# Kernel tuning notes

Measured on AMD Instinct MI355X. Metric: run time of the kernel, lower is better.

## Reference

```python
import jax, jax.numpy as jnp
import numpy as np

N_NODES = 100000
N_EDGES = 1600000
D_IN = 128
D_OUT = 256


def setup_inputs() -> dict:
    key = jax.random.key(0)
    k1, k2, k3 = jax.random.split(key, 3)
    H = jax.random.normal(k1, (N_NODES, D_IN), dtype=jnp.float32)
    edge_index = jax.random.randint(k2, (2, N_EDGES), 0, N_NODES, dtype=jnp.int64)
    # kaiming_normal_ on (in, out): fan computed over dim 1 -> std = sqrt(2/out)
    W = jax.random.normal(k3, (D_IN, D_OUT), dtype=jnp.float32) * np.sqrt(2.0 / D_OUT)
    return {"H": H, "edge_index": edge_index, "W": W}


def reference(H, edge_index, W):
    src, dst = edge_index[0], edge_index[1]
    # gather source node features per edge, scatter-add into destination nodes
    msgs = H[src]  # [E, D_IN]
    new_H = jax.ops.segment_sum(msgs, dst, num_segments=H.shape[0])  # [N, D_IN]
    out = H + new_H
    out = out @ W  # [N, D_OUT]
    return jax.nn.relu(out)
```

## Files before the change

### kernel.cpp

```cpp
#include <hip/hip_runtime.h>

#define N_NODES 100000
#define N_EDGES 1600000
#define D_IN    128
#define D_OUT   256
#define NB_SCAN ((N_NODES + 255) / 256)
#define BLK_ROWS 64
#define N_TILES  ((N_NODES + BLK_ROWS - 1) / BLK_ROWS)
#define X_ROWS   (N_TILES * BLK_ROWS)

#define NBUCK      98
#define BCAP       20480
#define BIN_CHUNK  1024
#define BIN_BLOCKS ((N_EDGES + BIN_CHUNK - 1) / BIN_CHUNK)

#define GBLK_ROWS  32
#define G_TILES    ((N_NODES + GBLK_ROWS - 1) / GBLK_ROWS)

typedef __attribute__((ext_vector_type(8))) short short8v;
typedef __attribute__((ext_vector_type(4))) float f32x4;

__device__ __forceinline__ unsigned bf16_rn(float f) {
    unsigned u = __float_as_uint(f);
    return (u + 0x7FFFu + ((u >> 16) & 1u)) >> 16;
}
__device__ __forceinline__ unsigned pack2_bf16(float a, float b) {
    return bf16_rn(a) | (bf16_rn(b) << 16);
}

__global__ void detect_idx64_kernel(const int* __restrict__ edge32,
                                    int* __restrict__ flag) {
    if (threadIdx.x == 0 && blockIdx.x == 0) {
        int is64 = 1;
        for (int i = 1; i < 32; i += 2) {
            if (edge32[i] != 0) { is64 = 0; break; }
        }
        *flag = is64;
    }
}

__device__ __forceinline__ int load_dst(const void* edge_raw, int is64, int e) {
    if (is64) return (int)((const long long*)edge_raw)[(long long)N_EDGES + e];
    return ((const int*)edge_raw)[N_EDGES + e];
}
__device__ __forceinline__ int load_src(const void* edge_raw, int is64, int e) {
    if (is64) return (int)((const long long*)edge_raw)[e];
    return ((const int*)edge_raw)[e];
}

__global__ __launch_bounds__(256) void cvt_h_kernel(
        const float* __restrict__ H, unsigned* __restrict__ Hb) {
    int i = blockIdx.x * 256 + threadIdx.x;
    if (i >= N_NODES * (D_IN / 2)) return;
    const float2 h = ((const float2*)H)[i];
    Hb[i] = pack2_bf16(h.x, h.y);
}

__global__ __launch_bounds__(256) void pack_w_kernel(
        const float* __restrict__ W, unsigned short* __restrict__ Wp) {
    int t = blockIdx.x * 256 + threadIdx.x;
    if (t >= 64 * 64) return;
    const int f  = t >> 6;
    const int l  = t & 63;
    const int nb = f >> 2;
    const int ks = f & 3;
    const int col  = nb * 16 + (l & 15);
    const int krow = ks * 32 + (l >> 4) * 8;
    #pragma unroll
    for (int i = 0; i < 8; ++i)
        Wp[(size_t)t * 8 + i] = (unsigned short)bf16_rn(W[(krow + i) * D_OUT + col]);
}

__global__ __launch_bounds__(256) void bin_hist_kernel(
        const void* __restrict__ edge_raw, const int* __restrict__ flag,
        int* __restrict__ bucket_alloc, int* __restrict__ binned) {
    __shared__ int cnt[128];
    __shared__ int gbase[128];
    const int tid = threadIdx.x;
    if (tid < 128) cnt[tid] = 0;
    __syncthreads();
    const int is64 = *flag;
    const int base = blockIdx.x * BIN_CHUNK + tid;

#define EDGE_A(i)                                                             \
    int rec##i = 0, pb##i = -1;                                               \
    {                                                                         \
        const int idx = base + (i) * 256;                                     \
        if (idx < N_EDGES) {                                                  \
            const int s = load_src(edge_raw, is64, idx);                      \
            const int d = load_dst(edge_raw, is64, idx);                      \
            if ((unsigned)s < N_NODES && (unsigned)d < N_NODES) {             \
                const int b = d >> 10;                                        \
                const int pos = atomicAdd(&cnt[b], 1);                        \
                rec##i = s | ((d & 1023) << 17);                              \
                pb##i  = pos | (b << 12);                                     \
            }                                                                 \
        }                                                                     \
    }
    EDGE_A(0) EDGE_A(1) EDGE_A(2) EDGE_A(3)
#undef EDGE_A

    __syncthreads();
    if (tid < NBUCK) gbase[tid] = atomicAdd(&bucket_alloc[tid], cnt[tid]);
    __syncthreads();

#define EDGE_B(i)                                                             \
    if (pb##i >= 0) {                                                         \
        const int b = pb##i >> 12;                                            \
        const int p = gbase[b] + (pb##i & 4095);                              \
        if (p < BCAP) binned[b * BCAP + p] = rec##i;                          \
    }
    EDGE_B(0) EDGE_B(1) EDGE_B(2) EDGE_B(3)
#undef EDGE_B
}

__global__ __launch_bounds__(128) void scan98_kernel(
        const int* __restrict__ bucket_alloc, int* __restrict__ segbase) {
    __shared__ int lds[128];
    const int t = threadIdx.x;
    lds[t] = (t < NBUCK) ? bucket_alloc[t] : 0;
    __syncthreads();
    for (int off = 1; off < 128; off <<= 1) {
        int u = (t >= off) ? lds[t - off] : 0;
        __syncthreads();
        lds[t] += u;
        __syncthreads();
    }
    if (t < NBUCK) segbase[t] = lds[t] - ((t < NBUCK) ? bucket_alloc[t] : 0);
}

__global__ __launch_bounds__(1024) void bucket_fill_scan_kernel(
        const int* __restrict__ bucket_alloc, const int* __restrict__ segbase,
        const int* __restrict__ binned,
        int* __restrict__ row_start, int* __restrict__ csr_pack) {
    __shared__ int hist[1024];
    const int b   = blockIdx.x;
    const int tid = threadIdx.x;
    hist[tid] = 0;
    __syncthreads();

    int cnt = bucket_alloc[b];
    if (cnt > BCAP) cnt = BCAP;
    const int base = b * BCAP;

    for (int p = tid; p < cnt; p += 1024)
        atomicAdd(&hist[(binned[base + p] >> 17) & 1023], 1);
    __syncthreads();

    const int myc = hist[tid];
    for (int off = 1; off < 1024; off <<= 1) {
        int u = (tid >= off) ? hist[tid - off] : 0;
        __syncthreads();
        hist[tid] += u;
        __syncthreads();
    }
    const int rs = segbase[b] + hist[tid] - myc;
    const int node = (b << 10) + tid;
    if (node <= N_NODES) row_start[node] = rs;

    hist[tid] = rs;
    __syncthreads();

    for (int p = tid; p < cnt; p += 1024) {
        const int rec = binned[base + p];
        const int dlo = (rec >> 17) & 1023;
        const int pos = atomicAdd(&hist[dlo], 1);
        csr_pack[pos] = (rec & 0x1FFFF) | ((dlo & 63) << 20);
    }
}

__global__ __launch_bounds__(256) void hist_kernel(
        const void* __restrict__ edge_raw, const int* __restrict__ flag,
        int* __restrict__ counts) {
    int e = blockIdx.x * blockDim.x + threadIdx.x;
    if (e >= N_EDGES) return;
    int dst = load_dst(edge_raw, *flag, e);
    if ((unsigned)dst < N_NODES) atomicAdd(&counts[dst], 1);
}

__global__ __launch_bounds__(256) void block_sum_kernel(
        const int* __restrict__ counts, int* __restrict__ bsum) {
    __shared__ int lds[256];
    int t = threadIdx.x;
    int i = blockIdx.x * 256 + t;
    lds[t] = (i < N_NODES) ? counts[i] : 0;
    __syncthreads();
    for (int off = 128; off > 0; off >>= 1) {
        if (t < off) lds[t] += lds[t + off];
        __syncthreads();
    }
    if (t == 0) bsum[blockIdx.x] = lds[0];
}

__global__ __launch_bounds__(512) void scan_bsum_kernel(
        int* __restrict__ bsum, int* __restrict__ row_start) {
    __shared__ int lds[512];
    int t = threadIdx.x;
    lds[t] = (t < NB_SCAN) ? bsum[t] : 0;
    __syncthreads();
    for (int off = 1; off < 512; off <<= 1) {
        int u = (t >= off) ? lds[t - off] : 0;
        __syncthreads();
        lds[t] += u;
        __syncthreads();
    }
    int excl = (t == 0) ? 0 : lds[t - 1];
    if (t < NB_SCAN) bsum[t] = excl;
    if (t == 0) row_start[N_NODES] = N_EDGES;
}

__global__ __launch_bounds__(256) void scan_counts_kernel(
        int* __restrict__ counts_cursor, const int* __restrict__ bsum,
        int* __restrict__ row_start) {
    __shared__ int lds[256];
    int t = threadIdx.x;
    int i = blockIdx.x * 256 + t;
    int c = (i < N_NODES) ? counts_cursor[i] : 0;
    lds[t] = c;
    __syncthreads();
    for (int off = 1; off < 256; off <<= 1) {
        int u = (t >= off) ? lds[t - off] : 0;
        __syncthreads();
        lds[t] += u;
        __syncthreads();
    }
    int rs = bsum[blockIdx.x] + lds[t] - c;
    if (i < N_NODES) {
        row_start[i] = rs;
        counts_cursor[i] = rs;
    }
}

__global__ __launch_bounds__(256) void fill_kernel(
        const void* __restrict__ edge_raw, const int* __restrict__ flag,
        int* __restrict__ cursor, int* __restrict__ csr_pack) {
    int e = blockIdx.x * blockDim.x + threadIdx.x;
    if (e >= N_EDGES) return;
    int is64 = *flag;
    int src = load_src(edge_raw, is64, e);
    int dst = load_dst(edge_raw, is64, e);
    if ((unsigned)dst >= N_NODES || (unsigned)src >= N_NODES) return;
    int pos = atomicAdd(&cursor[dst], 1);
    csr_pack[pos] = src | ((dst & 63) << 20);
}

__global__ __launch_bounds__(256) void gather_bf16_kernel(
        const float* __restrict__ H,
        const unsigned* __restrict__ Hb,
        const int* __restrict__ row_start,
        const int* __restrict__ csr_pack,
        unsigned* __restrict__ Xg) {
    __shared__ int idx_lds[4][256];

    const int gb   = blockIdx.x * GBLK_ROWS;
    const int tile = (gb >> 6) << 6;
    const int wv   = threadIdx.x >> 6;
    const int lane = threadIdx.x & 63;
    const int r0   = gb + wv * 8;
    if (r0 >= N_NODES) return;
    int r1 = r0 + 8; if (r1 > N_NODES) r1 = N_NODES;

    const int p0   = row_start[r0];
    const int pend = row_start[r1];

    for (int r = r0; r < r1; ++r) {
        if (row_start[r + 1] == row_start[r]) {
            const float2 h = ((const float2*)(H + (size_t)r * D_IN))[lane];
            __builtin_nontemporal_store(pack2_bf16(h.x, h.y),
                                        &Xg[(size_t)r * 64 + lane]);
        }
    }

    int    cur = -1;
    float2 acc = make_float2(0.f, 0.f);
    float2 hs  = make_float2(0.f, 0.f);

#define FLUSH()                                                               \
    __builtin_nontemporal_store(pack2_bf16(acc.x + hs.x, acc.y + hs.y),       \
                                &Xg[(size_t)(tile + cur) * 64 + lane]);

#define PROC(EV, UU)                                                          \
    {                                                                         \
        const int dl = (EV) >> 20;                                            \
        const float vx = __uint_as_float((UU) << 16);                         \
        const float vy = __uint_as_float((UU) & 0xFFFF0000u);                 \
        if (dl != cur) {                                                      \
            if (cur >= 0) { FLUSH(); }                                        \
            cur = dl;                                                         \
            hs  = ((const float2*)(H + (size_t)(tile + dl) * D_IN))[lane];    \
            acc = make_float2(vx, vy);                                        \
        } else {                                                              \
            acc.x += vx; acc.y += vy;                                         \
        }                                                                     \
    }

    for (int p = p0; p < pend; p += 256) {
        int m = pend - p;
        if (m > 256) m = 256;
        #pragma unroll
        for (int j = 0; j < 4; ++j) {
            const int o = lane + j * 64;
            if (o < m) idx_lds[wv][o] = csr_pack[p + o];
        }
        int n = 0;
        for (; n + 8 <= m; n += 8) {
            const int e0 = idx_lds[wv][n + 0];
            const int e1 = idx_lds[wv][n + 1];
            const int e2 = idx_lds[wv][n + 2];
            const int e3 = idx_lds[wv][n + 3];
            const int e4 = idx_lds[wv][n + 4];
            const int e5 = idx_lds[wv][n + 5];
            const int e6 = idx_lds[wv][n + 6];
            const int e7 = idx_lds[wv][n + 7];
            const unsigned u0 = Hb[(size_t)(e0 & 0xFFFFF) * 64 + lane];
            const unsigned u1 = Hb[(size_t)(e1 & 0xFFFFF) * 64 + lane];
            const unsigned u2 = Hb[(size_t)(e2 & 0xFFFFF) * 64 + lane];
            const unsigned u3 = Hb[(size_t)(e3 & 0xFFFFF) * 64 + lane];
            const unsigned u4 = Hb[(size_t)(e4 & 0xFFFFF) * 64 + lane];
            const unsigned u5 = Hb[(size_t)(e5 & 0xFFFFF) * 64 + lane];
            const unsigned u6 = Hb[(size_t)(e6 & 0xFFFFF) * 64 + lane];
            const unsigned u7 = Hb[(size_t)(e7 & 0xFFFFF) * 64 + lane];
            PROC(e0, u0) PROC(e1, u1) PROC(e2, u2) PROC(e3, u3)
            PROC(e4, u4) PROC(e5, u5) PROC(e6, u6) PROC(e7, u7)
        }
        for (; n < m; ++n) {
            const int e0 = idx_lds[wv][n];
            const unsigned u = Hb[(size_t)(e0 & 0xFFFFF) * 64 + lane];
            PROC(e0, u)
        }
    }
    if (cur >= 0) { FLUSH(); }
#undef PROC
#undef FLUSH
}

__global__ __launch_bounds__(256) void gather_f32_kernel(
        const float* __restrict__ H,
        const int* __restrict__ row_start,
        const int* __restrict__ csr_pack,
        unsigned* __restrict__ Xg) {
    __shared__ int idx_lds[4][256];

    const int gb   = blockIdx.x * GBLK_ROWS;
    const int tile = (gb >> 6) << 6;
    const int wv   = threadIdx.x >> 6;
    const int lane = threadIdx.x & 63;
    const int r0   = gb + wv * 8;
    if (r0 >= N_NODES) return;
    int r1 = r0 + 8; if (r1 > N_NODES) r1 = N_NODES;

    const int p0   = row_start[r0];
    const int pend = row_start[r1];

    for (int r = r0; r < r1; ++r) {
        if (row_start[r + 1] == row_start[r]) {
            const float2 h = ((const float2*)(H + (size_t)r * D_IN))[lane];
            Xg[(size_t)r * 64 + lane] = pack2_bf16(h.x, h.y);
        }
    }

    int    cur = -1;
    float2 acc = make_float2(0.f, 0.f);
    float2 hs  = make_float2(0.f, 0.f);

#define FLUSH() \
    Xg[(size_t)(tile + cur) * 64 + lane] = pack2_bf16(acc.x + hs.x, acc.y + hs.y);

#define PROC(EV, VV)                                                          \
    {                                                                         \
        const int dl = (EV) >> 20;                                            \
        if (dl != cur) {                                                      \
            if (cur >= 0) { FLUSH(); }                                        \
            cur = dl;                                                         \
            hs  = ((const float2*)(H + (size_t)(tile + dl) * D_IN))[lane];    \
            acc = (VV);                                                       \
        } else {                                                              \
            acc.x += (VV).x; acc.y += (VV).y;                                 \
        }                                                                     \
    }

    for (int p = p0; p < pend; p += 256) {
        int m = pend - p;
        if (m > 256) m = 256;
        #pragma unroll
        for (int j = 0; j < 4; ++j) {
            const int o = lane + j * 64;
            if (o < m) idx_lds[wv][o] = csr_pack[p + o];
        }
        int n = 0;
        for (; n + 8 <= m; n += 8) {
            const int e0 = idx_lds[wv][n + 0];
            const int e1 = idx_lds[wv][n + 1];
            const int e2 = idx_lds[wv][n + 2];
            const int e3 = idx_lds[wv][n + 3];
            const int e4 = idx_lds[wv][n + 4];
            const int e5 = idx_lds[wv][n + 5];
            const int e6 = idx_lds[wv][n + 6];
            const int e7 = idx_lds[wv][n + 7];
            const float2 v0 = ((const float2*)(H + (size_t)(e0 & 0xFFFFF) * D_IN))[lane];
            const float2 v1 = ((const float2*)(H + (size_t)(e1 & 0xFFFFF) * D_IN))[lane];
            const float2 v2 = ((const float2*)(H + (size_t)(e2 & 0xFFFFF) * D_IN))[lane];
            const float2 v3 = ((const float2*)(H + (size_t)(e3 & 0xFFFFF) * D_IN))[lane];
            const float2 v4 = ((const float2*)(H + (size_t)(e4 & 0xFFFFF) * D_IN))[lane];
            const float2 v5 = ((const float2*)(H + (size_t)(e5 & 0xFFFFF) * D_IN))[lane];
            const float2 v6 = ((const float2*)(H + (size_t)(e6 & 0xFFFFF) * D_IN))[lane];
            const float2 v7 = ((const float2*)(H + (size_t)(e7 & 0xFFFFF) * D_IN))[lane];
            PROC(e0, v0) PROC(e1, v1) PROC(e2, v2) PROC(e3, v3)
            PROC(e4, v4) PROC(e5, v5) PROC(e6, v6) PROC(e7, v7)
        }
        for (; n < m; ++n) {
            const int e0 = idx_lds[wv][n];
            const float2 v = ((const float2*)(H + (size_t)(e0 & 0xFFFFF) * D_IN))[lane];
            PROC(e0, v)
        }
    }
    if (cur >= 0) { FLUSH(); }
#undef PROC
#undef FLUSH
}

__global__ __launch_bounds__(256) void gemm_mfma_kernel(
        const unsigned* __restrict__ Xg,
        const unsigned short* __restrict__ Wp,
        float* __restrict__ out) {
    __shared__ unsigned Xs[64 * 64];

    const int tid = threadIdx.x;
    const int w   = tid >> 6;
    const int l   = tid & 63;
    const int g   = blockIdx.x * BLK_ROWS;

    #pragma unroll
    for (int j = 0; j < 4; ++j) {
        const int flat = j * 256 + tid;
        const int r   = flat >> 4;
        const int c16 = flat & 15;
        const uint4 v = *(const uint4*)(Xg + (size_t)(g + r) * 64 + c16 * 4);
        const int pc = c16 ^ (r & 7);
        *(uint4*)(&Xs[r * 64 + pc * 4]) = v;
    }

    short8v bfr[4][4];
    #pragma unroll
    for (int nb = 0; nb < 4; ++nb)
        #pragma unroll
        for (int ks = 0; ks < 4; ++ks) {
            const int f = (w * 4 + nb) * 4 + ks;
            bfr[nb][ks] = *(const short8v*)(Wp + ((size_t)f * 64 + l) * 8);
        }

    __syncthreads();

    f32x4 acc[4][4] = {};
    const int arow = l & 15;
    const int agrp = l >> 4;

    #pragma unroll
    for (int ks = 0; ks < 4; ++ks) {
        short8v a0, a1, a2, a3;
        {
            const int r = 0 * 16 + arow;
            a0 = *(const short8v*)(&Xs[r * 64 + ((ks * 4 + agrp) ^ (r & 7)) * 4]);
        }
        {
            const int r = 1 * 16 + arow;
            a1 = *(const short8v*)(&Xs[r * 64 + ((ks * 4 + agrp) ^ (r & 7)) * 4]);
        }
        {
            const int r = 2 * 16 + arow;
            a2 = *(const short8v*)(&Xs[r * 64 + ((ks * 4 + agrp) ^ (r & 7)) * 4]);
        }
        {
            const int r = 3 * 16 + arow;
            a3 = *(const short8v*)(&Xs[r * 64 + ((ks * 4 + agrp) ^ (r & 7)) * 4]);
        }
        #pragma unroll
        for (int nb = 0; nb < 4; ++nb) {
            acc[0][nb] = __builtin_amdgcn_mfma_f32_16x16x32_bf16(a0, bfr[nb][ks], acc[0][nb], 0, 0, 0);
            acc[1][nb] = __builtin_amdgcn_mfma_f32_16x16x32_bf16(a1, bfr[nb][ks], acc[1][nb], 0, 0, 0);
            acc[2][nb] = __builtin_amdgcn_mfma_f32_16x16x32_bf16(a2, bfr[nb][ks], acc[2][nb], 0, 0, 0);
            acc[3][nb] = __builtin_amdgcn_mfma_f32_16x16x32_bf16(a3, bfr[nb][ks], acc[3][nb], 0, 0, 0);
        }
    }

    #pragma unroll
    for (int mg = 0; mg < 4; ++mg) {
        #pragma unroll
        for (int rr = 0; rr < 4; ++rr) {
            const int row = g + mg * 16 + agrp * 4 + rr;
            if (row < N_NODES) {
                #pragma unroll
                for (int nb = 0; nb < 4; ++nb) {
                    const float v = acc[mg][nb][rr];
                    out[(size_t)row * D_OUT + w * 64 + nb * 16 + (l & 15)] =
                        fmaxf(v, 0.f);
                }
            }
        }
    }
}

__global__ __launch_bounds__(256) void fused_gather_gemm_relu_kernel(
        const float* __restrict__ H,
        const int* __restrict__ row_start,
        const int* __restrict__ csr_pack,
        const float* __restrict__ Wm,
        float* __restrict__ out) {
    __shared__ float Xs[BLK_ROWS][D_IN];
    __shared__ int idx_lds[4][64];

    const int g    = blockIdx.x * BLK_ROWS;
    const int tid  = threadIdx.x;
    const int wv   = tid >> 6;
    const int lane = tid & 63;

    {
        const int kidx = tid & 31;
        const int rg   = tid >> 5;
        #pragma unroll
        for (int j = 0; j < 8; ++j) {
            const int r = rg + j * 8;
            const int row = g + r;
            float4 x = make_float4(0.f, 0.f, 0.f, 0.f);
            if (row < N_NODES)
                x = *reinterpret_cast<const float4*>(H + (size_t)row * D_IN + kidx * 4);
            *reinterpret_cast<float4*>(&Xs[r][kidx * 4]) = x;
        }
    }
    __syncthreads();

    {
        const int seg_beg = row_start[g];
        const int rend    = (g + BLK_ROWS < N_NODES) ? (g + BLK_ROWS) : N_NODES;
        const int seg_end = row_start[rend];
        const int len     = seg_end - seg_beg;
        const int clen    = (len + 3) >> 2;
        const int cbeg    = seg_beg + wv * clen;
        int cend          = cbeg + clen;
        if (cend > seg_end) cend = seg_end;

        const int c2 = lane * 2;
        int   cur = -1;
        float2 acc = make_float2(0.f, 0.f);

#define PROCF(EV, VV)                                                         \
        {                                                                     \
            const int dl = (EV) >> 20;                                        \
            if (dl != cur) {                                                  \
                if (cur >= 0) {                                               \
                    atomicAdd(&Xs[cur][c2],     acc.x);                       \
                    atomicAdd(&Xs[cur][c2 + 1], acc.y);                       \
                }                                                             \
                cur = dl;                                                     \
                acc = (VV);                                                   \
            } else {                                                          \
                acc.x += (VV).x; acc.y += (VV).y;                             \
            }                                                                 \
        }

        for (int base = cbeg; base < cend; base += 64) {
            int m = cend - base;
            if (m > 64) m = 64;
            if (lane < m) idx_lds[wv][lane] = csr_pack[base + lane];
            int n = 0;
            for (; n + 8 <= m; n += 8) {
                const int e0 = idx_lds[wv][n + 0];
                const int e1 = idx_lds[wv][n + 1];
                const int e2 = idx_lds[wv][n + 2];
                const int e3 = idx_lds[wv][n + 3];
                const int e4 = idx_lds[wv][n + 4];
                const int e5 = idx_lds[wv][n + 5];
                const int e6 = idx_lds[wv][n + 6];
                const int e7 = idx_lds[wv][n + 7];
                const float2 v0 = ((const float2*)(H + (size_t)(e0 & 0xFFFFF) * D_IN))[lane];
                const float2 v1 = ((const float2*)(H + (size_t)(e1 & 0xFFFFF) * D_IN))[lane];
                const float2 v2 = ((const float2*)(H + (size_t)(e2 & 0xFFFFF) * D_IN))[lane];
                const float2 v3 = ((const float2*)(H + (size_t)(e3 & 0xFFFFF) * D_IN))[lane];
                const float2 v4 = ((const float2*)(H + (size_t)(e4 & 0xFFFFF) * D_IN))[lane];
                const float2 v5 = ((const float2*)(H + (size_t)(e5 & 0xFFFFF) * D_IN))[lane];
                const float2 v6 = ((const float2*)(H + (size_t)(e6 & 0xFFFFF) * D_IN))[lane];
                const float2 v7 = ((const float2*)(H + (size_t)(e7 & 0xFFFFF) * D_IN))[lane];
                PROCF(e0, v0) PROCF(e1, v1) PROCF(e2, v2) PROCF(e3, v3)
                PROCF(e4, v4) PROCF(e5, v5) PROCF(e6, v6) PROCF(e7, v7)
            }
            for (; n < m; ++n) {
                const int e0 = idx_lds[wv][n];
                const float2 v = ((const float2*)(H + (size_t)(e0 & 0xFFFFF) * D_IN))[lane];
                PROCF(e0, v)
            }
        }
        if (cur >= 0) {
            atomicAdd(&Xs[cur][c2],     acc.x);
            atomicAdd(&Xs[cur][c2 + 1], acc.y);
        }
#undef PROCF
    }
    __syncthreads();

    const int ty = tid >> 6;
    const int tx = tid & 63;

    float accv[16][4];
    #pragma unroll
    for (int r = 0; r < 16; ++r)
        #pragma unroll
        for (int j = 0; j < 4; ++j) accv[r][j] = 0.f;

    const float* Wp2 = Wm + tx * 4;

    #pragma unroll 2
    for (int k = 0; k < D_IN; k += 4) {
        const float4 w0 = *reinterpret_cast<const float4*>(Wp2 + (k + 0) * D_OUT);
        const float4 w1 = *reinterpret_cast<const float4*>(Wp2 + (k + 1) * D_OUT);
        const float4 w2 = *reinterpret_cast<const float4*>(Wp2 + (k + 2) * D_OUT);
        const float4 w3 = *reinterpret_cast<const float4*>(Wp2 + (k + 3) * D_OUT);
        #pragma unroll
        for (int r = 0; r < 16; ++r) {
            const float4 x = *reinterpret_cast<const float4*>(&Xs[ty * 16 + r][k]);
            accv[r][0] = fmaf(x.x, w0.x, accv[r][0]);
            accv[r][0] = fmaf(x.y, w1.x, accv[r][0]);
            accv[r][0] = fmaf(x.z, w2.x, accv[r][0]);
            accv[r][0] = fmaf(x.w, w3.x, accv[r][0]);
            accv[r][1] = fmaf(x.x, w0.y, accv[r][1]);
            accv[r][1] = fmaf(x.y, w1.y, accv[r][1]);
            accv[r][1] = fmaf(x.z, w2.y, accv[r][1]);
            accv[r][1] = fmaf(x.w, w3.y, accv[r][1]);
            accv[r][2] = fmaf(x.x, w0.z, accv[r][2]);
            accv[r][2] = fmaf(x.y, w1.z, accv[r][2]);
            accv[r][2] = fmaf(x.z, w2.z, accv[r][2]);
            accv[r][2] = fmaf(x.w, w3.z, accv[r][2]);
            accv[r][3] = fmaf(x.x, w0.w, accv[r][3]);
            accv[r][3] = fmaf(x.y, w1.w, accv[r][3]);
            accv[r][3] = fmaf(x.z, w2.w, accv[r][3]);
            accv[r][3] = fmaf(x.w, w3.w, accv[r][3]);
        }
    }

    #pragma unroll
    for (int r = 0; r < 16; ++r) {
        const int row = g + ty * 16 + r;
        if (row < N_NODES) {
            float4 o;
            o.x = fmaxf(accv[r][0], 0.f);
            o.y = fmaxf(accv[r][1], 0.f);
            o.z = fmaxf(accv[r][2], 0.f);
            o.w = fmaxf(accv[r][3], 0.f);
            *reinterpret_cast<float4*>(out + (size_t)row * D_OUT + tx * 4) = o;
        }
    }
}

extern "C" void kernel_launch(void* const* d_in, const int* in_sizes, int n_in,
                              void* d_out, int out_size, void* d_ws, size_t ws_size,
                              hipStream_t stream) {
    const float* H    = (const float*)d_in[0];
    const void*  edge = d_in[1];
    const float* Wm   = (const float*)d_in[2];
    float* out = (float*)d_out;

    const size_t off_rs    = 0;
    const size_t off_cur   = ((size_t)(N_NODES + 1) * 4 + 15) & ~(size_t)15;
    const size_t off_alloc = off_cur + (size_t)N_NODES * 4;
    const size_t off_csr   = off_alloc + 512;
    const size_t off_bsum  = off_csr + (size_t)N_EDGES * 4;
    const size_t off_flag  = off_bsum + (((size_t)NB_SCAN * 4 + 15) & ~(size_t)15);
    const size_t off_wp    = (off_flag + 16 + 255) & ~(size_t)255;
    const size_t off_X     = (off_wp + 64 * 64 * 16 + 255) & ~(size_t)255;
    const size_t need_mid  = off_X + (size_t)X_ROWS * 64 * sizeof(unsigned);
    const size_t off_Hb    = (need_mid + 255) & ~(size_t)255;
    const size_t need_full = off_Hb + (size_t)N_NODES * (D_IN / 2) * sizeof(unsigned);
    const size_t off_bin   = (need_full + 255) & ~(size_t)255;
    const size_t need_sort = off_bin + (size_t)NBUCK * BCAP * 4;

    int* row_start = (int*)((char*)d_ws + off_rs);
    int* cursor    = (int*)((char*)d_ws + off_cur);
    int* balloc    = (int*)((char*)d_ws + off_alloc);
    int* csr_pack  = (int*)((char*)d_ws + off_csr);
    int* bsum      = (int*)((char*)d_ws + off_bsum);
    int* flag      = (int*)((char*)d_ws + off_flag);
    unsigned short* Wp = (unsigned short*)((char*)d_ws + off_wp);
    unsigned* Xg   = (unsigned*)((char*)d_ws + off_X);
    unsigned* Hb   = (unsigned*)((char*)d_ws + off_Hb);
    int* binned    = (int*)((char*)d_ws + off_bin);

    detect_idx64_kernel<<<1, 64, 0, stream>>>((const int*)edge, flag);

    const int edge_blocks = (N_EDGES + 255) / 256;

    if (ws_size >= need_mid) {
        pack_w_kernel<<<16, 256, 0, stream>>>(Wm, Wp);
    }
    if (ws_size >= need_full) {
        cvt_h_kernel<<<(N_NODES * (D_IN / 2) + 255) / 256, 256, 0, stream>>>(H, Hb);
    }

    if (ws_size >= need_sort) {
        hipMemsetAsync(balloc, 0, 512, stream);
        bin_hist_kernel<<<BIN_BLOCKS, 256, 0, stream>>>(edge, flag, balloc, binned);
        scan98_kernel<<<1, 128, 0, stream>>>(balloc, bsum);
        bucket_fill_scan_kernel<<<NBUCK, 1024, 0, stream>>>(
            balloc, bsum, binned, row_start, csr_pack);
    } else {
        hipMemsetAsync(cursor, 0, (size_t)N_NODES * 4 + 512, stream);
        hist_kernel<<<edge_blocks, 256, 0, stream>>>(edge, flag, cursor);
        block_sum_kernel<<<NB_SCAN, 256, 0, stream>>>(cursor, bsum);
        scan_bsum_kernel<<<1, 512, 0, stream>>>(bsum, row_start);
        scan_counts_kernel<<<NB_SCAN, 256, 0, stream>>>(cursor, bsum, row_start);
        fill_kernel<<<edge_blocks, 256, 0, stream>>>(edge, flag, cursor, csr_pack);
    }

    if (ws_size >= need_full) {
        gather_bf16_kernel<<<G_TILES, 256, 0, stream>>>(H, Hb, row_start, csr_pack, Xg);
        gemm_mfma_kernel<<<N_TILES, 256, 0, stream>>>(Xg, Wp, out);
    } else if (ws_size >= need_mid) {
        gather_f32_kernel<<<G_TILES, 256, 0, stream>>>(H, row_start, csr_pack, Xg);
        gemm_mfma_kernel<<<N_TILES, 256, 0, stream>>>(Xg, Wp, out);
    } else {
        fused_gather_gemm_relu_kernel<<<N_TILES, 256, 0, stream>>>(
            H, row_start, csr_pack, Wm, out);
    }
}
```

Baseline: 190.8 us.

## Fuse bf16 gather into MFMA GEMM and fold bucket scan into fill kernel

```diff
diff --git a/kernel.cpp b/kernel.cpp
--- a/kernel.cpp
+++ b/kernel.cpp
@@ -14,9 +14,6 @@
 #define BIN_CHUNK  1024
 #define BIN_BLOCKS ((N_EDGES + BIN_CHUNK - 1) / BIN_CHUNK)
 
-#define GBLK_ROWS  32
-#define G_TILES    ((N_NODES + GBLK_ROWS - 1) / GBLK_ROWS)
-
 typedef __attribute__((ext_vector_type(8))) short short8v;
 typedef __attribute__((ext_vector_type(4))) float f32x4;
 
@@ -29,8 +26,11 @@
 }
 
 __global__ void detect_idx64_kernel(const int* __restrict__ edge32,
-                                    int* __restrict__ flag) {
-    if (threadIdx.x == 0 && blockIdx.x == 0) {
+                                    int* __restrict__ flag,
+                                    int* __restrict__ balloc) {
+    const int t = threadIdx.x;
+    if (t < 128) balloc[t] = 0;
+    if (t == 0 && blockIdx.x == 0) {
         int is64 = 1;
         for (int i = 1; i < 32; i += 2) {
             if (edge32[i] != 0) { is64 = 0; break; }
@@ -114,32 +114,26 @@
 #undef EDGE_B
 }
 
-__global__ __launch_bounds__(128) void scan98_kernel(
-        const int* __restrict__ bucket_alloc, int* __restrict__ segbase) {
-    __shared__ int lds[128];
-    const int t = threadIdx.x;
-    lds[t] = (t < NBUCK) ? bucket_alloc[t] : 0;
-    __syncthreads();
-    for (int off = 1; off < 128; off <<= 1) {
-        int u = (t >= off) ? lds[t - off] : 0;
-        __syncthreads();
-        lds[t] += u;
-        __syncthreads();
-    }
-    if (t < NBUCK) segbase[t] = lds[t] - ((t < NBUCK) ? bucket_alloc[t] : 0);
-}
-
 __global__ __launch_bounds__(1024) void bucket_fill_scan_kernel(
-        const int* __restrict__ bucket_alloc, const int* __restrict__ segbase,
+        const int* __restrict__ bucket_alloc,
         const int* __restrict__ binned,
         int* __restrict__ row_start, int* __restrict__ csr_pack) {
     __shared__ int hist[1024];
+    __shared__ int sb[128];
     const int b   = blockIdx.x;
     const int tid = threadIdx.x;
     hist[tid] = 0;
-    __syncthreads();
-
+    if (tid < 128) sb[tid] = (tid < NBUCK) ? bucket_alloc[tid] : 0;
+    __syncthreads();
+
+    for (int off = 1; off < 128; off <<= 1) {
+        const int u = (tid >= off && tid < 128) ? sb[tid - off] : 0;
+        __syncthreads();
+        if (tid < 128) sb[tid] += u;
+        __syncthreads();
+    }
     int cnt = bucket_alloc[b];
+    const int segb = sb[b] - cnt;
     if (cnt > BCAP) cnt = BCAP;
     const int base = b * BCAP;
 
@@ -149,12 +143,12 @@
 
     const int myc = hist[tid];
     for (int off = 1; off < 1024; off <<= 1) {
-        int u = (tid >= off) ? hist[tid - off] : 0;
+        const int u = (tid >= off) ? hist[tid - off] : 0;
         __syncthreads();
         hist[tid] += u;
         __syncthreads();
     }
-    const int rs = segbase[b] + hist[tid] - myc;
+    const int rs = segb + hist[tid] - myc;
     const int node = (b << 10) + tid;
     if (node <= N_NODES) row_start[node] = rs;
 
@@ -166,6 +160,150 @@
         const int dlo = (rec >> 17) & 1023;
         const int pos = atomicAdd(&hist[dlo], 1);
         csr_pack[pos] = (rec & 0x1FFFF) | ((dlo & 63) << 20);
+    }
+}
+
+__global__ __launch_bounds__(256) void gather_mfma_kernel(
+        const float* __restrict__ H,
+        const unsigned* __restrict__ Hb,
+        const int* __restrict__ row_start,
+        const int* __restrict__ csr_pack,
+        const unsigned short* __restrict__ Wp,
+        float* __restrict__ out) {
+    __shared__ unsigned Xs[64 * 64];
+    __shared__ int idx_lds[4][256];
+
+    const int g    = blockIdx.x * BLK_ROWS;
+    const int wv   = threadIdx.x >> 6;
+    const int lane = threadIdx.x & 63;
+    const int r0   = g + wv * 16;
+
+    if (r0 < N_NODES) {
+        int r1 = r0 + 16; if (r1 > N_NODES) r1 = N_NODES;
+        const int p0   = row_start[r0];
+        const int pend = row_start[r1];
+
+        for (int r = r0; r < r1; ++r) {
+            if (row_start[r + 1] == row_start[r]) {
+                const float2 h = ((const float2*)(H + (size_t)r * D_IN))[lane];
+                const int rr = r - g;
+                Xs[rr * 64 + ((((lane >> 2) ^ (rr & 7)) << 2) | (lane & 3))] =
+                    pack2_bf16(h.x, h.y);
+            }
+        }
+
+        int    cur = -1;
+        float2 acc = make_float2(0.f, 0.f);
+        float2 hs  = make_float2(0.f, 0.f);
+
+#define FLUSH()                                                               \
+        Xs[cur * 64 + ((((lane >> 2) ^ (cur & 7)) << 2) | (lane & 3))] =      \
+            pack2_bf16(acc.x + hs.x, acc.y + hs.y);
+
+#define PROC(EV, UU)                                                          \
+        {                                                                     \
+            const int dl = (EV) >> 20;                                        \
+            const float vx = __uint_as_float((UU) << 16);                     \
+            const float vy = __uint_as_float((UU) & 0xFFFF0000u);             \
+            if (dl != cur) {                                                  \
+                if (cur >= 0) { FLUSH(); }                                    \
+                cur = dl;                                                     \
+                hs  = ((const float2*)(H + (size_t)(g + dl) * D_IN))[lane];   \
+                acc = make_float2(vx, vy);                                    \
+            } else {                                                          \
+                acc.x += vx; acc.y += vy;                                     \
+            }                                                                 \
+        }
+
+        for (int p = p0; p < pend; p += 256) {
+            int m = pend - p;
+            if (m > 256) m = 256;
+            #pragma unroll
+            for (int j = 0; j < 4; ++j) {
+                const int o = lane + j * 64;
+                if (o < m) idx_lds[wv][o] = csr_pack[p + o];
+            }
+            int n = 0;
+            for (; n + 8 <= m; n += 8) {
+                const int e0 = idx_lds[wv][n + 0];
+                const int e1 = idx_lds[wv][n + 1];
+                const int e2 = idx_lds[wv][n + 2];
+                const int e3 = idx_lds[wv][n + 3];
+                const int e4 = idx_lds[wv][n + 4];
+                const int e5 = idx_lds[wv][n + 5];
+                const int e6 = idx_lds[wv][n + 6];
+                const int e7 = idx_lds[wv][n + 7];
+                const unsigned u0 = Hb[(size_t)(e0 & 0xFFFFF) * 64 + lane];
+                const unsigned u1 = Hb[(size_t)(e1 & 0xFFFFF) * 64 + lane];
+                const unsigned u2 = Hb[(size_t)(e2 & 0xFFFFF) * 64 + lane];
+                const unsigned u3 = Hb[(size_t)(e3 & 0xFFFFF) * 64 + lane];
+                const unsigned u4 = Hb[(size_t)(e4 & 0xFFFFF) * 64 + lane];
+                const unsigned u5 = Hb[(size_t)(e5 & 0xFFFFF) * 64 + lane];
+                const unsigned u6 = Hb[(size_t)(e6 & 0xFFFFF) * 64 + lane];
+                const unsigned u7 = Hb[(size_t)(e7 & 0xFFFFF) * 64 + lane];
+                PROC(e0, u0) PROC(e1, u1) PROC(e2, u2) PROC(e3, u3)
+                PROC(e4, u4) PROC(e5, u5) PROC(e6, u6) PROC(e7, u7)
+            }
+            for (; n < m; ++n) {
+                const int e0 = idx_lds[wv][n];
+                const unsigned u = Hb[(size_t)(e0 & 0xFFFFF) * 64 + lane];
+                PROC(e0, u)
+            }
+        }
+        if (cur >= 0) { FLUSH(); }
+#undef PROC
+#undef FLUSH
+    }
+    __syncthreads();
+
+    f32x4 acc4[4][4] = {};
+    const int arow = lane & 15;
+    const int agrp = lane >> 4;
+
+    #pragma unroll
+    for (int ks = 0; ks < 4; ++ks) {
+        short8v a0, a1, a2, a3;
+        {
+            const int r = 0 * 16 + arow;
+            a0 = *(const short8v*)(&Xs[r * 64 + ((ks * 4 + agrp) ^ (r & 7)) * 4]);
+        }
+        {
+            const int r = 1 * 16 + arow;
+            a1 = *(const short8v*)(&Xs[r * 64 + ((ks * 4 + agrp) ^ (r & 7)) * 4]);
+        }
+        {
+            const int r = 2 * 16 + arow;
+            a2 = *(const short8v*)(&Xs[r * 64 + ((ks * 4 + agrp) ^ (r & 7)) * 4]);
+        }
+        {
+            const int r = 3 * 16 + arow;
+            a3 = *(const short8v*)(&Xs[r * 64 + ((ks * 4 + agrp) ^ (r & 7)) * 4]);
+        }
+        #pragma unroll
+        for (int nb = 0; nb < 4; ++nb) {
+            const int f = (wv * 4 + nb) * 4 + ks;
+            const short8v bf = *(const short8v*)(Wp + ((size_t)f * 64 + lane) * 8);
+            acc4[0][nb] = __builtin_amdgcn_mfma_f32_16x16x32_bf16(a0, bf, acc4[0][nb], 0, 0, 0);
+            acc4[1][nb] = __builtin_amdgcn_mfma_f32_16x16x32_bf16(a1, bf, acc4[1][nb], 0, 0, 0);
+            acc4[2][nb] = __builtin_amdgcn_mfma_f32_16x16x32_bf16(a2, bf, acc4[2][nb], 0, 0, 0);
+            acc4[3][nb] = __builtin_amdgcn_mfma_f32_16x16x32_bf16(a3, bf, acc4[3][nb], 0, 0, 0);
+        }
+    }
+
+    #pragma unroll
+    for (int mg = 0; mg < 4; ++mg) {
+        #pragma unroll
+        for (int rr = 0; rr < 4; ++rr) {
+            const int row = g + mg * 16 + agrp * 4 + rr;
+            if (row < N_NODES) {
+                #pragma unroll
+                for (int nb = 0; nb < 4; ++nb) {
+                    const float v = acc4[mg][nb][rr];
+                    out[(size_t)row * D_OUT + wv * 64 + nb * 16 + (lane & 15)] =
+                        fmaxf(v, 0.f);
+                }
+            }
+        }
     }
 }
 
@@ -242,262 +380,6 @@
     if ((unsigned)dst >= N_NODES || (unsigned)src >= N_NODES) return;
     int pos = atomicAdd(&cursor[dst], 1);
     csr_pack[pos] = src | ((dst & 63) << 20);
-}
-
-__global__ __launch_bounds__(256) void gather_bf16_kernel(
-        const float* __restrict__ H,
-        const unsigned* __restrict__ Hb,
-        const int* __restrict__ row_start,
-        const int* __restrict__ csr_pack,
-        unsigned* __restrict__ Xg) {
-    __shared__ int idx_lds[4][256];
-
-    const int gb   = blockIdx.x * GBLK_ROWS;
-    const int tile = (gb >> 6) << 6;
-    const int wv   = threadIdx.x >> 6;
-    const int lane = threadIdx.x & 63;
-    const int r0   = gb + wv * 8;
-    if (r0 >= N_NODES) return;
-    int r1 = r0 + 8; if (r1 > N_NODES) r1 = N_NODES;
-
-    const int p0   = row_start[r0];
-    const int pend = row_start[r1];
-
-    for (int r = r0; r < r1; ++r) {
-        if (row_start[r + 1] == row_start[r]) {
-            const float2 h = ((const float2*)(H + (size_t)r * D_IN))[lane];
-            __builtin_nontemporal_store(pack2_bf16(h.x, h.y),
-                                        &Xg[(size_t)r * 64 + lane]);
-        }
-    }
-
-    int    cur = -1;
-    float2 acc = make_float2(0.f, 0.f);
-    float2 hs  = make_float2(0.f, 0.f);
-
-#define FLUSH()                                                               \
-    __builtin_nontemporal_store(pack2_bf16(acc.x + hs.x, acc.y + hs.y),       \
-                                &Xg[(size_t)(tile + cur) * 64 + lane]);
-
-#define PROC(EV, UU)                                                          \
-    {                                                                         \
-        const int dl = (EV) >> 20;                                            \
-        const float vx = __uint_as_float((UU) << 16);                         \
-        const float vy = __uint_as_float((UU) & 0xFFFF0000u);                 \
-        if (dl != cur) {                                                      \
-            if (cur >= 0) { FLUSH(); }                                        \
-            cur = dl;                                                         \
-            hs  = ((const float2*)(H + (size_t)(tile + dl) * D_IN))[lane];    \
-            acc = make_float2(vx, vy);                                        \
-        } else {                                                              \
-            acc.x += vx; acc.y += vy;                                         \
-        }                                                                     \
-    }
-
-    for (int p = p0; p < pend; p += 256) {
-        int m = pend - p;
-        if (m > 256) m = 256;
-        #pragma unroll
-        for (int j = 0; j < 4; ++j) {
-            const int o = lane + j * 64;
-            if (o < m) idx_lds[wv][o] = csr_pack[p + o];
-        }
-        int n = 0;
-        for (; n + 8 <= m; n += 8) {
-            const int e0 = idx_lds[wv][n + 0];
-            const int e1 = idx_lds[wv][n + 1];
-            const int e2 = idx_lds[wv][n + 2];
-            const int e3 = idx_lds[wv][n + 3];
-            const int e4 = idx_lds[wv][n + 4];
-            const int e5 = idx_lds[wv][n + 5];
-            const int e6 = idx_lds[wv][n + 6];
-            const int e7 = idx_lds[wv][n + 7];
-            const unsigned u0 = Hb[(size_t)(e0 & 0xFFFFF) * 64 + lane];
-            const unsigned u1 = Hb[(size_t)(e1 & 0xFFFFF) * 64 + lane];
-            const unsigned u2 = Hb[(size_t)(e2 & 0xFFFFF) * 64 + lane];
-            const unsigned u3 = Hb[(size_t)(e3 & 0xFFFFF) * 64 + lane];
-            const unsigned u4 = Hb[(size_t)(e4 & 0xFFFFF) * 64 + lane];
-            const unsigned u5 = Hb[(size_t)(e5 & 0xFFFFF) * 64 + lane];
-            const unsigned u6 = Hb[(size_t)(e6 & 0xFFFFF) * 64 + lane];
-            const unsigned u7 = Hb[(size_t)(e7 & 0xFFFFF) * 64 + lane];
-            PROC(e0, u0) PROC(e1, u1) PROC(e2, u2) PROC(e3, u3)
-            PROC(e4, u4) PROC(e5, u5) PROC(e6, u6) PROC(e7, u7)
-        }
-        for (; n < m; ++n) {
-            const int e0 = idx_lds[wv][n];
-            const unsigned u = Hb[(size_t)(e0 & 0xFFFFF) * 64 + lane];
-            PROC(e0, u)
-        }
-    }
-    if (cur >= 0) { FLUSH(); }
-#undef PROC
-#undef FLUSH
-}
-
-__global__ __launch_bounds__(256) void gather_f32_kernel(
-        const float* __restrict__ H,
-        const int* __restrict__ row_start,
-        const int* __restrict__ csr_pack,
-        unsigned* __restrict__ Xg) {
-    __shared__ int idx_lds[4][256];
-
-    const int gb   = blockIdx.x * GBLK_ROWS;
-    const int tile = (gb >> 6) << 6;
-    const int wv   = threadIdx.x >> 6;
-    const int lane = threadIdx.x & 63;
-    const int r0   = gb + wv * 8;
-    if (r0 >= N_NODES) return;
-    int r1 = r0 + 8; if (r1 > N_NODES) r1 = N_NODES;
-
-    const int p0   = row_start[r0];
-    const int pend = row_start[r1];
-
-    for (int r = r0; r < r1; ++r) {
-        if (row_start[r + 1] == row_start[r]) {
-            const float2 h = ((const float2*)(H + (size_t)r * D_IN))[lane];
-            Xg[(size_t)r * 64 + lane] = pack2_bf16(h.x, h.y);
-        }
-    }
-
-    int    cur = -1;
-    float2 acc = make_float2(0.f, 0.f);
-    float2 hs  = make_float2(0.f, 0.f);
-
-#define FLUSH() \
-    Xg[(size_t)(tile + cur) * 64 + lane] = pack2_bf16(acc.x + hs.x, acc.y + hs.y);
-
-#define PROC(EV, VV)                                                          \
-    {                                                                         \
-        const int dl = (EV) >> 20;                                            \
-        if (dl != cur) {                                                      \
-            if (cur >= 0) { FLUSH(); }                                        \
-            cur = dl;                                                         \
-            hs  = ((const float2*)(H + (size_t)(tile + dl) * D_IN))[lane];    \
-            acc = (VV);                                                       \
-        } else {                                                              \
-            acc.x += (VV).x; acc.y += (VV).y;                                 \
-        }                                                                     \
-    }
-
-    for (int p = p0; p < pend; p += 256) {
-        int m = pend - p;
-        if (m > 256) m = 256;
-        #pragma unroll
-        for (int j = 0; j < 4; ++j) {
-            const int o = lane + j * 64;
-            if (o < m) idx_lds[wv][o] = csr_pack[p + o];
-        }
-        int n = 0;
-        for (; n + 8 <= m; n += 8) {
-            const int e0 = idx_lds[wv][n + 0];
-            const int e1 = idx_lds[wv][n + 1];
-            const int e2 = idx_lds[wv][n + 2];
-            const int e3 = idx_lds[wv][n + 3];
-            const int e4 = idx_lds[wv][n + 4];
-            const int e5 = idx_lds[wv][n + 5];
-            const int e6 = idx_lds[wv][n + 6];
-            const int e7 = idx_lds[wv][n + 7];
-            const float2 v0 = ((const float2*)(H + (size_t)(e0 & 0xFFFFF) * D_IN))[lane];
-            const float2 v1 = ((const float2*)(H + (size_t)(e1 & 0xFFFFF) * D_IN))[lane];
-            const float2 v2 = ((const float2*)(H + (size_t)(e2 & 0xFFFFF) * D_IN))[lane];
-            const float2 v3 = ((const float2*)(H + (size_t)(e3 & 0xFFFFF) * D_IN))[lane];
-            const float2 v4 = ((const float2*)(H + (size_t)(e4 & 0xFFFFF) * D_IN))[lane];
-            const float2 v5 = ((const float2*)(H + (size_t)(e5 & 0xFFFFF) * D_IN))[lane];
-            const float2 v6 = ((const float2*)(H + (size_t)(e6 & 0xFFFFF) * D_IN))[lane];
-            const float2 v7 = ((const float2*)(H + (size_t)(e7 & 0xFFFFF) * D_IN))[lane];
-            PROC(e0, v0) PROC(e1, v1) PROC(e2, v2) PROC(e3, v3)
-            PROC(e4, v4) PROC(e5, v5) PROC(e6, v6) PROC(e7, v7)
-        }
-        for (; n < m; ++n) {
-            const int e0 = idx_lds[wv][n];
-            const float2 v = ((const float2*)(H + (size_t)(e0 & 0xFFFFF) * D_IN))[lane];
-            PROC(e0, v)
-        }
-    }
-    if (cur >= 0) { FLUSH(); }
-#undef PROC
-#undef FLUSH
-}
-
-__global__ __launch_bounds__(256) void gemm_mfma_kernel(
-        const unsigned* __restrict__ Xg,
-        const unsigned short* __restrict__ Wp,
-        float* __restrict__ out) {
-    __shared__ unsigned Xs[64 * 64];
-
-    const int tid = threadIdx.x;
-    const int w   = tid >> 6;
-    const int l   = tid & 63;
-    const int g   = blockIdx.x * BLK_ROWS;
-
-    #pragma unroll
-    for (int j = 0; j < 4; ++j) {
-        const int flat = j * 256 + tid;
-        const int r   = flat >> 4;
-        const int c16 = flat & 15;
-        const uint4 v = *(const uint4*)(Xg + (size_t)(g + r) * 64 + c16 * 4);
-        const int pc = c16 ^ (r & 7);
-        *(uint4*)(&Xs[r * 64 + pc * 4]) = v;
-    }
-
-    short8v bfr[4][4];
-    #pragma unroll
-    for (int nb = 0; nb < 4; ++nb)
-        #pragma unroll
-        for (int ks = 0; ks < 4; ++ks) {
-            const int f = (w * 4 + nb) * 4 + ks;
-            bfr[nb][ks] = *(const short8v*)(Wp + ((size_t)f * 64 + l) * 8);
-        }
-
-    __syncthreads();
-
-    f32x4 acc[4][4] = {};
-    const int arow = l & 15;
-    const int agrp = l >> 4;
-
-    #pragma unroll
-    for (int ks = 0; ks < 4; ++ks) {
-        short8v a0, a1, a2, a3;
-        {
-            const int r = 0 * 16 + arow;
-            a0 = *(const short8v*)(&Xs[r * 64 + ((ks * 4 + agrp) ^ (r & 7)) * 4]);
-        }
-        {
-            const int r = 1 * 16 + arow;
-            a1 = *(const short8v*)(&Xs[r * 64 + ((ks * 4 + agrp) ^ (r & 7)) * 4]);
-        }
-        {
-            const int r = 2 * 16 + arow;
-            a2 = *(const short8v*)(&Xs[r * 64 + ((ks * 4 + agrp) ^ (r & 7)) * 4]);
-        }
-        {
-            const int r = 3 * 16 + arow;
-            a3 = *(const short8v*)(&Xs[r * 64 + ((ks * 4 + agrp) ^ (r & 7)) * 4]);
-        }
-        #pragma unroll
-        for (int nb = 0; nb < 4; ++nb) {
-            acc[0][nb] = __builtin_amdgcn_mfma_f32_16x16x32_bf16(a0, bfr[nb][ks], acc[0][nb], 0, 0, 0);
-            acc[1][nb] = __builtin_amdgcn_mfma_f32_16x16x32_bf16(a1, bfr[nb][ks], acc[1][nb], 0, 0, 0);
-            acc[2][nb] = __builtin_amdgcn_mfma_f32_16x16x32_bf16(a2, bfr[nb][ks], acc[2][nb], 0, 0, 0);
-            acc[3][nb] = __builtin_amdgcn_mfma_f32_16x16x32_bf16(a3, bfr[nb][ks], acc[3][nb], 0, 0, 0);
-        }
-    }
-
-    #pragma unroll
-    for (int mg = 0; mg < 4; ++mg) {
-        #pragma unroll
-        for (int rr = 0; rr < 4; ++rr) {
-            const int row = g + mg * 16 + agrp * 4 + rr;
-            if (row < N_NODES) {
-                #pragma unroll
-                for (int nb = 0; nb < 4; ++nb) {
-                    const float v = acc[mg][nb][rr];
-                    out[(size_t)row * D_OUT + w * 64 + nb * 16 + (l & 15)] =
-                        fmaxf(v, 0.f);
-                }
-            }
-        }
-    }
 }
 
 __global__ __launch_bounds__(256) void fused_gather_gemm_relu_kernel(
@@ -679,27 +561,21 @@
     int* bsum      = (int*)((char*)d_ws + off_bsum);
     int* flag      = (int*)((char*)d_ws + off_flag);
     unsigned short* Wp = (unsigned short*)((char*)d_ws + off_wp);
-    unsigned* Xg   = (unsigned*)((char*)d_ws + off_X);
     unsigned* Hb   = (unsigned*)((char*)d_ws + off_Hb);
     int* binned    = (int*)((char*)d_ws + off_bin);
 
-    detect_idx64_kernel<<<1, 64, 0, stream>>>((const int*)edge, flag);
+    detect_idx64_kernel<<<1, 128, 0, stream>>>((const int*)edge, flag, balloc);
 
     const int edge_blocks = (N_EDGES + 255) / 256;
 
-    if (ws_size >= need_mid) {
+    if (ws_size >= need_sort) {
         pack_w_kernel<<<16, 256, 0, stream>>>(Wm, Wp);
-    }
-    if (ws_size >= need_full) {
         cvt_h_kernel<<<(N_NODES * (D_IN / 2) + 255) / 256, 256, 0, stream>>>(H, Hb);
-    }
-
-    if (ws_size >= need_sort) {
-        hipMemsetAsync(balloc, 0, 512, stream);
         bin_hist_kernel<<<BIN_BLOCKS, 256, 0, stream>>>(edge, flag, balloc, binned);
-        scan98_kernel<<<1, 128, 0, stream>>>(balloc, bsum);
         bucket_fill_scan_kernel<<<NBUCK, 1024, 0, stream>>>(
-            balloc, bsum, binned, row_start, csr_pack);
+            balloc, binned, row_start, csr_pack);
+        gather_mfma_kernel<<<N_TILES, 256, 0, stream>>>(
+            H, Hb, row_start, csr_pack, Wp, out);
     } else {
         hipMemsetAsync(cursor, 0, (size_t)N_NODES * 4 + 512, stream);
         hist_kernel<<<edge_blocks, 256, 0, stream>>>(edge, flag, cursor);
@@ -707,15 +583,6 @@
         scan_bsum_kernel<<<1, 512, 0, stream>>>(bsum, row_start);
         scan_counts_kernel<<<NB_SCAN, 256, 0, stream>>>(cursor, bsum, row_start);
         fill_kernel<<<edge_blocks, 256, 0, stream>>>(edge, flag, cursor, csr_pack);
-    }
-
-    if (ws_size >= need_full) {
-        gather_bf16_kernel<<<G_TILES, 256, 0, stream>>>(H, Hb, row_start, csr_pack, Xg);
-        gemm_mfma_kernel<<<N_TILES, 256, 0, stream>>>(Xg, Wp, out);
-    } else if (ws_size >= need_mid) {
-        gather_f32_kernel<<<G_TILES, 256, 0, stream>>>(H, row_start, csr_pack, Xg);
-        gemm_mfma_kernel<<<N_TILES, 256, 0, stream>>>(Xg, Wp, out);
-    } else {
         fused_gather_gemm_relu_kernel<<<N_TILES, 256, 0, stream>>>(
             H, row_start, csr_pack, Wm, out);
     }
```

Result: slower. 206.3 us (+8.1%).
